# Kernel optimization log

Measured on AMD Instinct MI355X. Metric: run time of the kernel, lower is better.

## Reference

```python
import jax, jax.numpy as jnp
import numpy as np

B, S, V, E, H, L = 16, 256, 32000, 512, 1024, 2


def setup_inputs() -> dict:
    key = jax.random.key(0)
    ks = jax.random.split(key, 10)
    scale = 0.02
    tokens = jax.random.randint(ks[0], (B, S), 1, V)  # avoid pad token 0
    emb = jax.random.normal(ks[1], (V, E), dtype=jnp.float32) * scale
    W0 = jax.random.normal(ks[2], (E, 4 * H), dtype=jnp.float32) * scale
    U0 = jax.random.normal(ks[3], (H, 4 * H), dtype=jnp.float32) * scale
    b0 = jnp.zeros((4 * H,), dtype=jnp.float32)
    W1 = jax.random.normal(ks[4], (H, 4 * H), dtype=jnp.float32) * scale
    U1 = jax.random.normal(ks[5], (H, 4 * H), dtype=jnp.float32) * scale
    b1 = jnp.zeros((4 * H,), dtype=jnp.float32)
    Wd = jax.random.normal(ks[6], (H, V), dtype=jnp.float32) * scale
    bd = jnp.zeros((V,), dtype=jnp.float32)
    return {"tokens": tokens, "emb": emb, "W0": W0, "U0": U0, "b0": b0,
            "W1": W1, "U1": U1, "b1": b1, "Wd": Wd, "bd": bd}


def lstm_layer(x, mask, W, U, b):
    """Keras LSTM (gate order i,f,g,o), mask carries state/output on padded steps.
    x: [B,S,D], mask: [B,S] bool -> (ys [B,S,H], h [B,H], c [B,H])."""
    h_dim = U.shape[0]
    bsz = x.shape[0]
    x_t = jnp.swapaxes(x, 0, 1)           # [S,B,D]
    m_t = jnp.swapaxes(mask, 0, 1)        # [S,B]

    def step(carry, inp):
        h, c = carry
        xt, mt = inp
        z = xt @ W + h @ U + b            # [B,4H]
        i, f, g, o = jnp.split(z, 4, axis=-1)
        c_new = jax.nn.sigmoid(f) * c + jax.nn.sigmoid(i) * jnp.tanh(g)
        h_new = jax.nn.sigmoid(o) * jnp.tanh(c_new)
        mt = mt[:, None]
        h_new = jnp.where(mt, h_new, h)
        c_new = jnp.where(mt, c_new, c)
        return (h_new, c_new), h_new

    init = (jnp.zeros((bsz, h_dim), x.dtype), jnp.zeros((bsz, h_dim), x.dtype))
    (h, c), ys = jax.lax.scan(step, init, (x_t, m_t))
    return jnp.swapaxes(ys, 0, 1), h, c


def reference(tokens, emb, W0, U0, b0, W1, U1, b1, Wd, bd):
    mask = tokens != 0                    # mask_zero=True in Embedding
    x = emb[tokens]                       # [B,S,E]
    x, h0, c0 = lstm_layer(x, mask, W0, U0, b0)
    x, h1, c1 = lstm_layer(x, mask, W1, U1, b1)
    probs = jax.nn.softmax(x @ Wd + bd, axis=-1)  # Dense(softmax) -> [B,S,V]
    h_stack = jnp.stack([h0, h1])         # [L,B,H] final hidden states
    c_stack = jnp.stack([c0, c1])         # [L,B,H] final cell states
    return probs, h_stack, c_stack
```

## Files before the change

kernel.cpp:

```cpp
#include <hip/hip_runtime.h>

typedef __attribute__((ext_vector_type(8))) short bf16x8;
typedef __attribute__((ext_vector_type(4))) float f32x4;

#define S_LEN 256
#define VOCAB 32000
#define EMB   512
#define HID   1024

static const size_t OUT_H = 131072000ull;

__device__ inline unsigned short f2bf(float f) {
  unsigned int u = __float_as_uint(f);
  u = (u + 0x7FFFu + ((u >> 16) & 1u)) >> 16;
  return (unsigned short)u;
}

__device__ inline void st_h(unsigned short* p, unsigned short v) {
  __hip_atomic_store(p, v, __ATOMIC_RELAXED, __HIP_MEMORY_SCOPE_AGENT);
}

__device__ inline int xcd_swz(int o, int n) {
  int q = n >> 3, r = n & 7;
  int x = o & 7, i = o >> 3;
  return (x < r ? x * (q + 1) : r * (q + 1) + (x - r) * q) + i;
}

__global__ __launch_bounds__(256) void k_transpose_bf16(const float* __restrict__ src,
                                                        unsigned short* __restrict__ dst,
                                                        int K, int N) {
  __shared__ float tile[64][65];
  int n0 = blockIdx.x * 64, k0 = blockIdx.y * 64;
  int tid = threadIdx.x;
#pragma unroll
  for (int i = 0; i < 16; ++i) {
    int e = tid + i * 256;
    int r = e >> 6, c = e & 63;
    tile[r][c] = src[(size_t)(k0 + r) * N + n0 + c];
  }
  __syncthreads();
#pragma unroll
  for (int i = 0; i < 16; ++i) {
    int e = tid + i * 256;
    int r = e >> 6, c = e & 63;
    dst[(size_t)(n0 + r) * K + k0 + c] = f2bf(tile[c][r]);
  }
}

__global__ __launch_bounds__(256) void k_gather_emb(const int* __restrict__ tokens,
                                                    const float* __restrict__ emb,
                                                    unsigned short* __restrict__ Xg) {
  int r = blockIdx.x;
  int s = r >> 4, b = r & 15;
  int tok = tokens[b * S_LEN + s];
  const float* src = emb + (size_t)tok * EMB;
  int k = threadIdx.x * 2;
  float2 v = *(const float2*)(src + k);
  ushort2 o; o.x = f2bf(v.x); o.y = f2bf(v.y);
  *(ushort2*)(Xg + (size_t)r * EMB + k) = o;
}

__device__ inline void gload16(const void* g, void* lds) {
  __builtin_amdgcn_global_load_lds((const __attribute__((address_space(1))) unsigned int*)g,
                                   (__attribute__((address_space(3))) unsigned int*)lds,
                                   16, 0, 0);
}

template <bool SMPART>
__global__ __launch_bounds__(256) void k_gemm_bf16(const unsigned short* __restrict__ A,
                                                   const unsigned short* __restrict__ BT,
                                                   float* __restrict__ C,
                                                   const float* __restrict__ bias,
                                                   int M, int N, int K,
                                                   float* __restrict__ Mpart,
                                                   float* __restrict__ Spart,
                                                   int NT) {
  __shared__ unsigned short As[4096];
  __shared__ unsigned short Bs[4096];
  __shared__ float redM[2][2][64];
  __shared__ float redS[2][2][64];
  int tid = threadIdx.x;
  int lane = tid & 63, wv = tid >> 6;
  int wr = wv >> 1, wc = wv & 1;
  int bxs = xcd_swz(blockIdx.x, gridDim.x);
  int am0 = blockIdx.y * 128, bn0 = bxs * 128;
  f32x4 zero = {0.f, 0.f, 0.f, 0.f};
  f32x4 acc[4][4];
#pragma unroll
  for (int m = 0; m < 4; ++m)
#pragma unroll
    for (int n = 0; n < 4; ++n) acc[m][n] = zero;
  int KT = K >> 5;
  int lr = lane & 15, kq = lane >> 4;
  for (int kt = 0; kt < KT; ++kt) {
    int k0 = kt << 5;
    __syncthreads();
#pragma unroll
    for (int c = 0; c < 2; ++c) {
      int t2 = c * 256 + tid;
      int row = t2 & 127, kg = t2 >> 7;
      gload16(A + (size_t)(am0 + row) * K + k0 + kg * 8, &As[(c * 256 + wv * 64) * 8]);
    }
#pragma unroll
    for (int c = 0; c < 2; ++c) {
      int t2 = c * 256 + tid;
      int row = t2 & 127, kg = t2 >> 7;
      gload16(BT + (size_t)(bn0 + row) * K + k0 + kg * 8, &Bs[(c * 256 + wv * 64) * 8]);
    }
    __syncthreads();
    const bf16x8* Ap = (const bf16x8*)As;
    const bf16x8* Bp = (const bf16x8*)Bs;
    bf16x8 af[4], bf[4];
#pragma unroll
    for (int m = 0; m < 4; ++m) af[m] = Ap[kq * 128 + wr * 64 + m * 16 + lr];
#pragma unroll
    for (int n = 0; n < 4; ++n) bf[n] = Bp[kq * 128 + wc * 64 + n * 16 + lr];
#pragma unroll
    for (int m = 0; m < 4; ++m)
#pragma unroll
      for (int n = 0; n < 4; ++n)
        acc[m][n] = __builtin_amdgcn_mfma_f32_16x16x32_bf16(af[m], bf[n], acc[m][n], 0, 0, 0);
  }
  float bvc[4];
#pragma unroll
  for (int n = 0; n < 4; ++n) {
    int col = bn0 + wc * 64 + n * 16 + lr;
    bvc[n] = bias ? bias[col] : 0.f;
  }
#pragma unroll
  for (int m = 0; m < 4; ++m)
#pragma unroll
    for (int n = 0; n < 4; ++n) {
      int col = bn0 + wc * 64 + n * 16 + lr;
#pragma unroll
      for (int q = 0; q < 4; ++q) {
        int row = am0 + wr * 64 + m * 16 + kq * 4 + q;
        C[(size_t)row * N + col] = acc[m][n][q] + bvc[n];
      }
    }
  if constexpr (SMPART) {
#pragma unroll
    for (int m = 0; m < 4; ++m)
#pragma unroll
      for (int q = 0; q < 4; ++q) {
        float mx = fmaxf(fmaxf(acc[m][0][q] + bvc[0], acc[m][1][q] + bvc[1]),
                         fmaxf(acc[m][2][q] + bvc[2], acc[m][3][q] + bvc[3]));
#pragma unroll
        for (int off = 1; off < 16; off <<= 1) mx = fmaxf(mx, __shfl_xor(mx, off));
        if (lr == 0) redM[wr][wc][m * 16 + kq * 4 + q] = mx;
      }
    __syncthreads();
#pragma unroll
    for (int m = 0; m < 4; ++m)
#pragma unroll
      for (int q = 0; q < 4; ++q) {
        int idx = m * 16 + kq * 4 + q;
        float mxF = fmaxf(redM[wr][0][idx], redM[wr][1][idx]);
        float s = __expf(acc[m][0][q] + bvc[0] - mxF) + __expf(acc[m][1][q] + bvc[1] - mxF) +
                  __expf(acc[m][2][q] + bvc[2] - mxF) + __expf(acc[m][3][q] + bvc[3] - mxF);
#pragma unroll
        for (int off = 1; off < 16; off <<= 1) s += __shfl_xor(s, off);
        if (lr == 0) redS[wr][wc][idx] = s;
      }
    __syncthreads();
    if (wc == 0 && lr == 0) {
#pragma unroll
      for (int m = 0; m < 4; ++m)
#pragma unroll
        for (int q = 0; q < 4; ++q) {
          int idx = m * 16 + kq * 4 + q;
          int row = am0 + wr * 64 + idx;
          Mpart[(size_t)row * NT + bxs] = fmaxf(redM[wr][0][idx], redM[wr][1][idx]);
          Spart[(size_t)row * NT + bxs] = redS[wr][0][idx] + redS[wr][1][idx];
        }
    }
  }
}

__global__ __launch_bounds__(256) void k_sm_combine(const float* __restrict__ Mp,
                                                    const float* __restrict__ Sp,
                                                    float* __restrict__ MS, int T) {
  int row = blockIdx.x * 4 + (threadIdx.x >> 6);
  int lane = threadIdx.x & 63;
  float mx = -3.4e38f;
  for (int i = lane; i < T; i += 64) mx = fmaxf(mx, Mp[(size_t)row * T + i]);
#pragma unroll
  for (int o = 32; o > 0; o >>= 1) mx = fmaxf(mx, __shfl_xor(mx, o));
  float s = 0.f;
  for (int i = lane; i < T; i += 64)
    s += Sp[(size_t)row * T + i] * __expf(Mp[(size_t)row * T + i] - mx);
#pragma unroll
  for (int o = 32; o > 0; o >>= 1) s += __shfl_xor(s, o);
  if (lane == 0) { MS[row * 2] = mx; MS[row * 2 + 1] = 1.f / s; }
}

__global__ __launch_bounds__(256) void k_sm_apply(float* __restrict__ data,
                                                  const float* __restrict__ MS) {
  const int total = 4096 * (VOCAB / 4);
  for (int idx = blockIdx.x * 256 + threadIdx.x; idx < total; idx += gridDim.x * 256) {
    int row = idx / (VOCAB / 4);
    float M = MS[row * 2], inv = MS[row * 2 + 1];
    float4 v = ((const float4*)data)[idx];
    v.x = __expf(v.x - M) * inv;
    v.y = __expf(v.y - M) * inv;
    v.z = __expf(v.z - M) * inv;
    v.w = __expf(v.w - M) * inv;
    ((float4*)data)[idx] = v;
  }
}

struct LstmSmem {
  unsigned short U0s[16384];
  unsigned short W1s[16384];
  unsigned short U1s[16384];
  float zA[4][16][16];
  float zB[4][16][16];
  float c0[16][4], h0f[16][4], c1[16][4], h1f[16][4];
  float b1s[16];
  short toks[16][256];
};

__global__ __launch_bounds__(256, 1) void k_lstm(const int* __restrict__ tokens,
                                                 const float* __restrict__ XW,
                                                 const unsigned short* __restrict__ U0T,
                                                 const unsigned short* __restrict__ W1T,
                                                 const unsigned short* __restrict__ U1T,
                                                 const float* __restrict__ b1,
                                                 unsigned short* __restrict__ h0r,
                                                 unsigned short* __restrict__ h1r,
                                                 unsigned short* __restrict__ Y1,
                                                 float* outHC,
                                                 int* bar) {
  extern __shared__ char smraw[];
  LstmSmem& sm = *(LstmSmem*)smraw;
  int tid = threadIdx.x, bid = blockIdx.x;
  int lane = tid & 63, wv = tid >> 6;

  for (int idx = tid; idx < 2048; idx += 256) {
    int cidx = idx >> 7, kg = idx & 127;
    int gcol = (cidx >> 2) * 1024 + bid * 4 + (cidx & 3);
    *(uint4*)&sm.U0s[(kg * 16 + cidx) * 8] = *(const uint4*)&U0T[(size_t)gcol * 1024 + kg * 8];
    *(uint4*)&sm.W1s[(kg * 16 + cidx) * 8] = *(const uint4*)&W1T[(size_t)gcol * 1024 + kg * 8];
    *(uint4*)&sm.U1s[(kg * 16 + cidx) * 8] = *(const uint4*)&U1T[(size_t)gcol * 1024 + kg * 8];
  }
  for (int idx = tid; idx < 4096; idx += 256) {
    sm.toks[idx >> 8][idx & 255] = (short)tokens[idx];
  }
  if (tid < 64) {
    int b = tid >> 2, u = tid & 3;
    sm.c0[b][u] = 0.f; sm.h0f[b][u] = 0.f;
    sm.c1[b][u] = 0.f; sm.h1f[b][u] = 0.f;
  }
  if (tid < 16) sm.b1s[tid] = b1[(tid >> 2) * 1024 + bid * 4 + (tid & 3)];
  __syncthreads();

  int lr = lane & 15, kq = lane >> 4;

  auto gbar = [&](int gen) {
    __syncthreads();
    if (tid == 0)
      __hip_atomic_store(&bar[bid * 16], gen, __ATOMIC_RELAXED, __HIP_MEMORY_SCOPE_AGENT);
    int ok;
    do {
      int f = __hip_atomic_load(&bar[tid * 16], __ATOMIC_RELAXED, __HIP_MEMORY_SCOPE_AGENT);
      ok = (f >= gen);
    } while (!__syncthreads_and(ok));
  };

  if (wv == 1) {
    int l = tid - 64, b = l >> 2, u = l & 3;
    const float* xp = XW + (size_t)b * 4096 + bid * 4 + u;
    float z0 = xp[0], z1 = xp[1024], z2 = xp[2048], z3 = xp[3072];
    (void)z1;
    float ii = 1.f / (1.f + expf(-z0));
    float gg = tanhf(z2);
    float oo = 1.f / (1.f + expf(-z3));
    float cn = ii * gg;
    float hn = oo * tanhf(cn);
    if (sm.toks[b][0] == 0) { cn = 0.f; hn = 0.f; }
    sm.c0[b][u] = cn; sm.h0f[b][u] = hn;
    st_h(h0r + b * HID + bid * 4 + u, f2bf(hn));
  }
  gbar(1);

  for (int t = 0; t < 255; ++t) {
    const unsigned short* h0t = h0r + (size_t)t * 16384;
    const unsigned short* h1p = h1r + (size_t)(t > 0 ? t - 1 : 0) * 16384;
    unsigned short* h1c = h1r + (size_t)t * 16384;
    unsigned short* h0n = h0r + (size_t)(t + 1) * 16384;

    float xwv0 = 0, xwv1 = 0, xwv2 = 0, xwv3 = 0;
    if (wv == 1) {
      int l = tid - 64, b = l >> 2, u = l & 3;
      const float* xp = XW + ((size_t)(t + 1) * 16 + b) * 4096 + bid * 4 + u;
      xwv0 = xp[0]; xwv1 = xp[1024]; xwv2 = xp[2048]; xwv3 = xp[3072];
    }

    f32x4 accB = {0.f, 0.f, 0.f, 0.f};
    {
      const unsigned short* ap = (wv < 2) ? h0t : h1p;
      const unsigned short* bm = (wv < 2) ? sm.W1s : sm.U1s;
      int kofs = (wv & 1) * 512;
      if (wv < 2 || t > 0) {
#pragma unroll
        for (int s8 = 0; s8 < 16; ++s8) {
          int kb = kofs + s8 * 32;
          bf16x8 av = *(const bf16x8*)(ap + lr * HID + kb + kq * 8);
          bf16x8 bv = *(const bf16x8*)&bm[(((kb >> 3) + kq) * 16 + lr) * 8];
          accB = __builtin_amdgcn_mfma_f32_16x16x32_bf16(av, bv, accB, 0, 0, 0);
        }
      }
    }
    f32x4 accA = {0.f, 0.f, 0.f, 0.f};
#pragma unroll
    for (int s8 = 0; s8 < 8; ++s8) {
      int kb = wv * 256 + s8 * 32;
      bf16x8 av = *(const bf16x8*)(h0t + lr * HID + kb + kq * 8);
      bf16x8 bv = *(const bf16x8*)&sm.U0s[(((kb >> 3) + kq) * 16 + lr) * 8];
      accA = __builtin_amdgcn_mfma_f32_16x16x32_bf16(av, bv, accA, 0, 0, 0);
    }
#pragma unroll
    for (int q = 0; q < 4; ++q) {
      sm.zB[wv][kq * 4 + q][lr] = accB[q];
      sm.zA[wv][kq * 4 + q][lr] = accA[q];
    }
    __syncthreads();

    if (wv == 0) {
      int b = tid >> 2, u = tid & 3;
      int tok = sm.toks[b][t];
      float z0 = sm.b1s[0 + u]  + sm.zB[0][b][0 + u]  + sm.zB[1][b][0 + u]  + sm.zB[2][b][0 + u]  + sm.zB[3][b][0 + u];
      float z1 = sm.b1s[4 + u]  + sm.zB[0][b][4 + u]  + sm.zB[1][b][4 + u]  + sm.zB[2][b][4 + u]  + sm.zB[3][b][4 + u];
      float z2 = sm.b1s[8 + u]  + sm.zB[0][b][8 + u]  + sm.zB[1][b][8 + u]  + sm.zB[2][b][8 + u]  + sm.zB[3][b][8 + u];
      float z3 = sm.b1s[12 + u] + sm.zB[0][b][12 + u] + sm.zB[1][b][12 + u] + sm.zB[2][b][12 + u] + sm.zB[3][b][12 + u];
      float ii = 1.f / (1.f + expf(-z0));
      float ff = 1.f / (1.f + expf(-z1));
      float gg = tanhf(z2);
      float oo = 1.f / (1.f + expf(-z3));
      float cold = sm.c1[b][u], hold = sm.h1f[b][u];
      float cn = ff * cold + ii * gg;
      float hn = oo * tanhf(cn);
      if (tok == 0) { cn = cold; hn = hold; }
      sm.c1[b][u] = cn; sm.h1f[b][u] = hn;
      unsigned short hb = f2bf(hn);
      st_h(h1c + b * HID + bid * 4 + u, hb);
      Y1[((size_t)b * S_LEN + t) * HID + bid * 4 + u] = hb;
    } else if (wv == 1) {
      int l = tid - 64, b = l >> 2, u = l & 3;
      int tok = sm.toks[b][t + 1];
      float z0 = xwv0 + sm.zA[0][b][0 + u]  + sm.zA[1][b][0 + u]  + sm.zA[2][b][0 + u]  + sm.zA[3][b][0 + u];
      float z1 = xwv1 + sm.zA[0][b][4 + u]  + sm.zA[1][b][4 + u]  + sm.zA[2][b][4 + u]  + sm.zA[3][b][4 + u];
      float z2 = xwv2 + sm.zA[0][b][8 + u]  + sm.zA[1][b][8 + u]  + sm.zA[2][b][8 + u]  + sm.zA[3][b][8 + u];
      float z3 = xwv3 + sm.zA[0][b][12 + u] + sm.zA[1][b][12 + u] + sm.zA[2][b][12 + u] + sm.zA[3][b][12 + u];
      float ii = 1.f / (1.f + expf(-z0));
      float ff = 1.f / (1.f + expf(-z1));
      float gg = tanhf(z2);
      float oo = 1.f / (1.f + expf(-z3));
      float cold = sm.c0[b][u], hold = sm.h0f[b][u];
      float cn = ff * cold + ii * gg;
      float hn = oo * tanhf(cn);
      if (tok == 0) { cn = cold; hn = hold; }
      sm.c0[b][u] = cn; sm.h0f[b][u] = hn;
      st_h(h0n + b * HID + bid * 4 + u, f2bf(hn));
    }
    gbar(t + 2);
  }

  {
    const unsigned short* h0t = h0r + 255ull * 16384;
    const unsigned short* h1p = h1r + 254ull * 16384;
    f32x4 accB = {0.f, 0.f, 0.f, 0.f};
    const unsigned short* ap = (wv < 2) ? h0t : h1p;
    const unsigned short* bm = (wv < 2) ? sm.W1s : sm.U1s;
    int kofs = (wv & 1) * 512;
#pragma unroll
    for (int s8 = 0; s8 < 16; ++s8) {
      int kb = kofs + s8 * 32;
      bf16x8 av = *(const bf16x8*)(ap + lr * HID + kb + kq * 8);
      bf16x8 bv = *(const bf16x8*)&bm[(((kb >> 3) + kq) * 16 + lr) * 8];
      accB = __builtin_amdgcn_mfma_f32_16x16x32_bf16(av, bv, accB, 0, 0, 0);
    }
#pragma unroll
    for (int q = 0; q < 4; ++q) sm.zB[wv][kq * 4 + q][lr] = accB[q];
    __syncthreads();
    if (wv == 0) {
      int b = tid >> 2, u = tid & 3;
      int tok = sm.toks[b][255];
      float z0 = sm.b1s[0 + u]  + sm.zB[0][b][0 + u]  + sm.zB[1][b][0 + u]  + sm.zB[2][b][0 + u]  + sm.zB[3][b][0 + u];
      float z1 = sm.b1s[4 + u]  + sm.zB[0][b][4 + u]  + sm.zB[1][b][4 + u]  + sm.zB[2][b][4 + u]  + sm.zB[3][b][4 + u];
      float z2 = sm.b1s[8 + u]  + sm.zB[0][b][8 + u]  + sm.zB[1][b][8 + u]  + sm.zB[2][b][8 + u]  + sm.zB[3][b][8 + u];
      float z3 = sm.b1s[12 + u] + sm.zB[0][b][12 + u] + sm.zB[1][b][12 + u] + sm.zB[2][b][12 + u] + sm.zB[3][b][12 + u];
      float ii = 1.f / (1.f + expf(-z0));
      float ff = 1.f / (1.f + expf(-z1));
      float gg = tanhf(z2);
      float oo = 1.f / (1.f + expf(-z3));
      float cold = sm.c1[b][u], hold = sm.h1f[b][u];
      float cn = ff * cold + ii * gg;
      float hn = oo * tanhf(cn);
      if (tok == 0) { cn = cold; hn = hold; }
      sm.c1[b][u] = cn; sm.h1f[b][u] = hn;
      Y1[((size_t)b * S_LEN + 255) * HID + bid * 4 + u] = f2bf(hn);
    }
    __syncthreads();
  }

  if (tid < 64) {
    int b = tid >> 2, u = tid & 3, ug = bid * 4 + u;
    outHC[OUT_H + (size_t)b * HID + ug]         = sm.h0f[b][u];
    outHC[OUT_H + 16384 + (size_t)b * HID + ug] = sm.h1f[b][u];
    outHC[OUT_H + 32768 + (size_t)b * HID + ug] = sm.c0[b][u];
    outHC[OUT_H + 49152 + (size_t)b * HID + ug] = sm.c1[b][u];
  }
}

extern "C" void kernel_launch(void* const* d_in, const int* in_sizes, int n_in,
                              void* d_out, int out_size, void* d_ws, size_t ws_size,
                              hipStream_t stream) {
  const int*   tokens = (const int*)d_in[0];
  const float* emb = (const float*)d_in[1];
  const float* W0  = (const float*)d_in[2];
  const float* U0  = (const float*)d_in[3];
  const float* b0  = (const float*)d_in[4];
  const float* W1  = (const float*)d_in[5];
  const float* U1  = (const float*)d_in[6];
  const float* b1  = (const float*)d_in[7];
  const float* Wd  = (const float*)d_in[8];
  const float* bd  = (const float*)d_in[9];
  float* out = (float*)d_out;

  char* ws = (char*)d_ws;
  size_t off = 0;
  auto alloc = [&](size_t bytes) { char* p = ws + off; off += (bytes + 255) & ~(size_t)255; return p; };
  unsigned short* W0T = (unsigned short*)alloc(4096ull * 512 * 2);
  unsigned short* U0T = (unsigned short*)alloc(4096ull * 1024 * 2);
  unsigned short* W1T = (unsigned short*)alloc(4096ull * 1024 * 2);
  unsigned short* U1T = (unsigned short*)alloc(4096ull * 1024 * 2);
  unsigned short* WdT = (unsigned short*)alloc(32000ull * 1024 * 2);
  unsigned short* Xg  = (unsigned short*)alloc(4096ull * 512 * 2);
  unsigned short* Y1  = (unsigned short*)alloc(4096ull * 1024 * 2);
  int*   bar   = (int*)alloc(16384);
  float* Mpart = (float*)alloc(4096ull * 250 * 4);
  float* Spart = (float*)alloc(4096ull * 250 * 4);
  float* MS    = (float*)alloc(4096ull * 2 * 4);

  float* XW = out;
  unsigned short* h0r = (unsigned short*)((char*)d_out + 192ull * 1024 * 1024);
  unsigned short* h1r = (unsigned short*)((char*)d_out + 208ull * 1024 * 1024);

  hipMemsetAsync(bar, 0, 16384, stream);

  hipFuncSetAttribute((const void*)k_lstm, hipFuncAttributeMaxDynamicSharedMemorySize,
                      (int)sizeof(LstmSmem));

  k_transpose_bf16<<<dim3(64, 8), 256, 0, stream>>>(W0, W0T, 512, 4096);
  k_transpose_bf16<<<dim3(64, 16), 256, 0, stream>>>(U0, U0T, 1024, 4096);
  k_transpose_bf16<<<dim3(64, 16), 256, 0, stream>>>(W1, W1T, 1024, 4096);
  k_transpose_bf16<<<dim3(64, 16), 256, 0, stream>>>(U1, U1T, 1024, 4096);
  k_transpose_bf16<<<dim3(500, 16), 256, 0, stream>>>(Wd, WdT, 1024, 32000);
  k_gather_emb<<<4096, 256, 0, stream>>>(tokens, emb, Xg);

  k_gemm_bf16<false><<<dim3(32, 32), 256, 0, stream>>>(Xg, W0T, XW, b0, 4096, 4096, 512,
                                                       nullptr, nullptr, 0);

  k_lstm<<<256, 256, sizeof(LstmSmem), stream>>>(tokens, XW, U0T, W1T, U1T, b1,
                                                 h0r, h1r, Y1, out, bar);

  k_gemm_bf16<true><<<dim3(250, 32), 256, 0, stream>>>(Y1, WdT, out, bd, 4096, 32000, 1024,
                                                       Mpart, Spart, 250);
  k_sm_combine<<<1024, 256, 0, stream>>>(Mpart, Spart, MS, 250);
  k_sm_apply<<<4096, 256, 0, stream>>>(out, MS);
}
```

Measured before the change: 2.423 ms.

## Split LSTM recurrence into two batch-half phases and store logits in bf16

The persistent LSTM kernel now handles the batch as two halves of 8 rows, each with its own grid-wide flag array. One half's compute can then overlap with other blocks still publishing the other half, which loosens the single global barrier per timestep. The MFMA A-operand rows are folded (r8) so each phase reads only 8 batch rows. Separately, when the workspace is large enough, the vocab GEMM writes bf16 logits to a scratch buffer and a new softmax-apply kernel reads them back, halving the logits round-trip traffic at the cost of bf16 rounding of the logits before exponentiation.

```diff
diff --git a/kernel.cpp b/kernel.cpp
--- a/kernel.cpp
+++ b/kernel.cpp
@@ -14,6 +14,9 @@
   unsigned int u = __float_as_uint(f);
   u = (u + 0x7FFFu + ((u >> 16) & 1u)) >> 16;
   return (unsigned short)u;
+}
+__device__ inline float bf2f(unsigned short s) {
+  return __uint_as_float(((unsigned int)s) << 16);
 }
 
 __device__ inline void st_h(unsigned short* p, unsigned short v) {
@@ -66,10 +69,11 @@
                                    16, 0, 0);
 }
 
-template <bool SMPART>
+template <bool SMPART, bool BF16OUT>
 __global__ __launch_bounds__(256) void k_gemm_bf16(const unsigned short* __restrict__ A,
                                                    const unsigned short* __restrict__ BT,
-                                                   float* __restrict__ C,
+                                                   float* __restrict__ Cf,
+                                                   unsigned short* __restrict__ Cb,
                                                    const float* __restrict__ bias,
                                                    int M, int N, int K,
                                                    float* __restrict__ Mpart,
@@ -135,7 +139,10 @@
 #pragma unroll
       for (int q = 0; q < 4; ++q) {
         int row = am0 + wr * 64 + m * 16 + kq * 4 + q;
-        C[(size_t)row * N + col] = acc[m][n][q] + bvc[n];
+        if constexpr (BF16OUT)
+          Cb[(size_t)row * N + col] = f2bf(acc[m][n][q] + bvc[n]);
+        else
+          Cf[(size_t)row * N + col] = acc[m][n][q] + bvc[n];
       }
     }
   if constexpr (SMPART) {
@@ -206,6 +213,23 @@
     v.z = __expf(v.z - M) * inv;
     v.w = __expf(v.w - M) * inv;
     ((float4*)data)[idx] = v;
+  }
+}
+
+__global__ __launch_bounds__(256) void k_sm_apply_bf16(const unsigned short* __restrict__ lg,
+                                                       float* __restrict__ probs,
+                                                       const float* __restrict__ MS) {
+  const int total = 4096 * (VOCAB / 4);
+  for (int idx = blockIdx.x * 256 + threadIdx.x; idx < total; idx += gridDim.x * 256) {
+    int row = idx / (VOCAB / 4);
+    float M = MS[row * 2], inv = MS[row * 2 + 1];
+    ushort4 v = ((const ushort4*)lg)[idx];
+    float4 o;
+    o.x = __expf(bf2f(v.x) - M) * inv;
+    o.y = __expf(bf2f(v.y) - M) * inv;
+    o.z = __expf(bf2f(v.z) - M) * inv;
+    o.w = __expf(bf2f(v.w) - M) * inv;
+    ((float4*)probs)[idx] = o;
   }
 }
 
@@ -255,14 +279,19 @@
   __syncthreads();
 
   int lr = lane & 15, kq = lane >> 4;
-
-  auto gbar = [&](int gen) {
+  int r8 = lane & 7;
+  int* flag0 = bar;
+  int* flag1 = bar + 4096;
+
+  auto publish = [&](int* base, int gen) {
     __syncthreads();
     if (tid == 0)
-      __hip_atomic_store(&bar[bid * 16], gen, __ATOMIC_RELAXED, __HIP_MEMORY_SCOPE_AGENT);
+      __hip_atomic_store(&base[bid * 16], gen, __ATOMIC_RELAXED, __HIP_MEMORY_SCOPE_AGENT);
+  };
+  auto wait_flags = [&](int* base, int gen) {
     int ok;
     do {
-      int f = __hip_atomic_load(&bar[tid * 16], __ATOMIC_RELAXED, __HIP_MEMORY_SCOPE_AGENT);
+      int f = __hip_atomic_load(&base[tid * 16], __ATOMIC_RELAXED, __HIP_MEMORY_SCOPE_AGENT);
       ok = (f >= gen);
     } while (!__syncthreads_and(ok));
   };
@@ -270,8 +299,7 @@
   if (wv == 1) {
     int l = tid - 64, b = l >> 2, u = l & 3;
     const float* xp = XW + (size_t)b * 4096 + bid * 4 + u;
-    float z0 = xp[0], z1 = xp[1024], z2 = xp[2048], z3 = xp[3072];
-    (void)z1;
+    float z0 = xp[0], z2 = xp[2048], z3 = xp[3072];
     float ii = 1.f / (1.f + expf(-z0));
     float gg = tanhf(z2);
     float oo = 1.f / (1.f + expf(-z3));
@@ -281,17 +309,18 @@
     sm.c0[b][u] = cn; sm.h0f[b][u] = hn;
     st_h(h0r + b * HID + bid * 4 + u, f2bf(hn));
   }
-  gbar(1);
-
-  for (int t = 0; t < 255; ++t) {
-    const unsigned short* h0t = h0r + (size_t)t * 16384;
-    const unsigned short* h1p = h1r + (size_t)(t > 0 ? t - 1 : 0) * 16384;
-    unsigned short* h1c = h1r + (size_t)t * 16384;
-    unsigned short* h0n = h0r + (size_t)(t + 1) * 16384;
+  publish(flag0, 1);
+  publish(flag1, 1);
+
+  auto phase = [&](int ph, int t) {
+    const unsigned short* h0t = h0r + (size_t)t * 16384 + ph * 8192;
+    const unsigned short* h1p = h1r + (size_t)(t > 0 ? t - 1 : 0) * 16384 + ph * 8192;
+    unsigned short* h1c = h1r + (size_t)t * 16384 + ph * 8192;
+    unsigned short* h0n = h0r + (size_t)(t + 1) * 16384 + ph * 8192;
 
     float xwv0 = 0, xwv1 = 0, xwv2 = 0, xwv3 = 0;
-    if (wv == 1) {
-      int l = tid - 64, b = l >> 2, u = l & 3;
+    if (wv == 1 && lane < 32) {
+      int b = ph * 8 + (lane >> 2), u = lane & 3;
       const float* xp = XW + ((size_t)(t + 1) * 16 + b) * 4096 + bid * 4 + u;
       xwv0 = xp[0]; xwv1 = xp[1024]; xwv2 = xp[2048]; xwv3 = xp[3072];
     }
@@ -305,7 +334,7 @@
 #pragma unroll
         for (int s8 = 0; s8 < 16; ++s8) {
           int kb = kofs + s8 * 32;
-          bf16x8 av = *(const bf16x8*)(ap + lr * HID + kb + kq * 8);
+          bf16x8 av = *(const bf16x8*)(ap + r8 * HID + kb + kq * 8);
           bf16x8 bv = *(const bf16x8*)&bm[(((kb >> 3) + kq) * 16 + lr) * 8];
           accB = __builtin_amdgcn_mfma_f32_16x16x32_bf16(av, bv, accB, 0, 0, 0);
         }
@@ -315,7 +344,7 @@
 #pragma unroll
     for (int s8 = 0; s8 < 8; ++s8) {
       int kb = wv * 256 + s8 * 32;
-      bf16x8 av = *(const bf16x8*)(h0t + lr * HID + kb + kq * 8);
+      bf16x8 av = *(const bf16x8*)(h0t + r8 * HID + kb + kq * 8);
       bf16x8 bv = *(const bf16x8*)&sm.U0s[(((kb >> 3) + kq) * 16 + lr) * 8];
       accA = __builtin_amdgcn_mfma_f32_16x16x32_bf16(av, bv, accA, 0, 0, 0);
     }
@@ -326,13 +355,13 @@
     }
     __syncthreads();
 
-    if (wv == 0) {
-      int b = tid >> 2, u = tid & 3;
+    if (tid < 32) {
+      int bl = tid >> 2, u = tid & 3, b = ph * 8 + bl;
       int tok = sm.toks[b][t];
-      float z0 = sm.b1s[0 + u]  + sm.zB[0][b][0 + u]  + sm.zB[1][b][0 + u]  + sm.zB[2][b][0 + u]  + sm.zB[3][b][0 + u];
-      float z1 = sm.b1s[4 + u]  + sm.zB[0][b][4 + u]  + sm.zB[1][b][4 + u]  + sm.zB[2][b][4 + u]  + sm.zB[3][b][4 + u];
-      float z2 = sm.b1s[8 + u]  + sm.zB[0][b][8 + u]  + sm.zB[1][b][8 + u]  + sm.zB[2][b][8 + u]  + sm.zB[3][b][8 + u];
-      float z3 = sm.b1s[12 + u] + sm.zB[0][b][12 + u] + sm.zB[1][b][12 + u] + sm.zB[2][b][12 + u] + sm.zB[3][b][12 + u];
+      float z0 = sm.b1s[0 + u]  + sm.zB[0][bl][0 + u]  + sm.zB[1][bl][0 + u]  + sm.zB[2][bl][0 + u]  + sm.zB[3][bl][0 + u];
+      float z1 = sm.b1s[4 + u]  + sm.zB[0][bl][4 + u]  + sm.zB[1][bl][4 + u]  + sm.zB[2][bl][4 + u]  + sm.zB[3][bl][4 + u];
+      float z2 = sm.b1s[8 + u]  + sm.zB[0][bl][8 + u]  + sm.zB[1][bl][8 + u]  + sm.zB[2][bl][8 + u]  + sm.zB[3][bl][8 + u];
+      float z3 = sm.b1s[12 + u] + sm.zB[0][bl][12 + u] + sm.zB[1][bl][12 + u] + sm.zB[2][bl][12 + u] + sm.zB[3][bl][12 + u];
       float ii = 1.f / (1.f + expf(-z0));
       float ff = 1.f / (1.f + expf(-z1));
       float gg = tanhf(z2);
@@ -343,15 +372,15 @@
       if (tok == 0) { cn = cold; hn = hold; }
       sm.c1[b][u] = cn; sm.h1f[b][u] = hn;
       unsigned short hb = f2bf(hn);
-      st_h(h1c + b * HID + bid * 4 + u, hb);
+      st_h(h1c + bl * HID + bid * 4 + u, hb);
       Y1[((size_t)b * S_LEN + t) * HID + bid * 4 + u] = hb;
-    } else if (wv == 1) {
-      int l = tid - 64, b = l >> 2, u = l & 3;
+    } else if (wv == 1 && lane < 32) {
+      int bl = lane >> 2, u = lane & 3, b = ph * 8 + bl;
       int tok = sm.toks[b][t + 1];
-      float z0 = xwv0 + sm.zA[0][b][0 + u]  + sm.zA[1][b][0 + u]  + sm.zA[2][b][0 + u]  + sm.zA[3][b][0 + u];
-      float z1 = xwv1 + sm.zA[0][b][4 + u]  + sm.zA[1][b][4 + u]  + sm.zA[2][b][4 + u]  + sm.zA[3][b][4 + u];
-      float z2 = xwv2 + sm.zA[0][b][8 + u]  + sm.zA[1][b][8 + u]  + sm.zA[2][b][8 + u]  + sm.zA[3][b][8 + u];
-      float z3 = xwv3 + sm.zA[0][b][12 + u] + sm.zA[1][b][12 + u] + sm.zA[2][b][12 + u] + sm.zA[3][b][12 + u];
+      float z0 = xwv0 + sm.zA[0][bl][0 + u]  + sm.zA[1][bl][0 + u]  + sm.zA[2][bl][0 + u]  + sm.zA[3][bl][0 + u];
+      float z1 = xwv1 + sm.zA[0][bl][4 + u]  + sm.zA[1][bl][4 + u]  + sm.zA[2][bl][4 + u]  + sm.zA[3][bl][4 + u];
+      float z2 = xwv2 + sm.zA[0][bl][8 + u]  + sm.zA[1][bl][8 + u]  + sm.zA[2][bl][8 + u]  + sm.zA[3][bl][8 + u];
+      float z3 = xwv3 + sm.zA[0][bl][12 + u] + sm.zA[1][bl][12 + u] + sm.zA[2][bl][12 + u] + sm.zA[3][bl][12 + u];
       float ii = 1.f / (1.f + expf(-z0));
       float ff = 1.f / (1.f + expf(-z1));
       float gg = tanhf(z2);
@@ -361,14 +390,22 @@
       float hn = oo * tanhf(cn);
       if (tok == 0) { cn = cold; hn = hold; }
       sm.c0[b][u] = cn; sm.h0f[b][u] = hn;
-      st_h(h0n + b * HID + bid * 4 + u, f2bf(hn));
-    }
-    gbar(t + 2);
-  }
-
-  {
-    const unsigned short* h0t = h0r + 255ull * 16384;
-    const unsigned short* h1p = h1r + 254ull * 16384;
+      st_h(h0n + bl * HID + bid * 4 + u, f2bf(hn));
+    }
+  };
+
+  for (int t = 0; t < 255; ++t) {
+    wait_flags(flag0, t + 1);
+    phase(0, t);
+    publish(flag0, t + 2);
+    wait_flags(flag1, t + 1);
+    phase(1, t);
+    publish(flag1, t + 2);
+  }
+
+  auto phaseEp = [&](int ph) {
+    const unsigned short* h0t = h0r + 255ull * 16384 + ph * 8192;
+    const unsigned short* h1p = h1r + 254ull * 16384 + ph * 8192;
     f32x4 accB = {0.f, 0.f, 0.f, 0.f};
     const unsigned short* ap = (wv < 2) ? h0t : h1p;
     const unsigned short* bm = (wv < 2) ? sm.W1s : sm.U1s;
@@ -376,20 +413,20 @@
 #pragma unroll
     for (int s8 = 0; s8 < 16; ++s8) {
       int kb = kofs + s8 * 32;
-      bf16x8 av = *(const bf16x8*)(ap + lr * HID + kb + kq * 8);
+      bf16x8 av = *(const bf16x8*)(ap + r8 * HID + kb + kq * 8);
       bf16x8 bv = *(const bf16x8*)&bm[(((kb >> 3) + kq) * 16 + lr) * 8];
       accB = __builtin_amdgcn_mfma_f32_16x16x32_bf16(av, bv, accB, 0, 0, 0);
     }
 #pragma unroll
     for (int q = 0; q < 4; ++q) sm.zB[wv][kq * 4 + q][lr] = accB[q];
     __syncthreads();
-    if (wv == 0) {
-      int b = tid >> 2, u = tid & 3;
+    if (tid < 32) {
+      int bl = tid >> 2, u = tid & 3, b = ph * 8 + bl;
       int tok = sm.toks[b][255];
-      float z0 = sm.b1s[0 + u]  + sm.zB[0][b][0 + u]  + sm.zB[1][b][0 + u]  + sm.zB[2][b][0 + u]  + sm.zB[3][b][0 + u];
-      float z1 = sm.b1s[4 + u]  + sm.zB[0][b][4 + u]  + sm.zB[1][b][4 + u]  + sm.zB[2][b][4 + u]  + sm.zB[3][b][4 + u];
-      float z2 = sm.b1s[8 + u]  + sm.zB[0][b][8 + u]  + sm.zB[1][b][8 + u]  + sm.zB[2][b][8 + u]  + sm.zB[3][b][8 + u];
-      float z3 = sm.b1s[12 + u] + sm.zB[0][b][12 + u] + sm.zB[1][b][12 + u] + sm.zB[2][b][12 + u] + sm.zB[3][b][12 + u];
+      float z0 = sm.b1s[0 + u]  + sm.zB[0][bl][0 + u]  + sm.zB[1][bl][0 + u]  + sm.zB[2][bl][0 + u]  + sm.zB[3][bl][0 + u];
+      float z1 = sm.b1s[4 + u]  + sm.zB[0][bl][4 + u]  + sm.zB[1][bl][4 + u]  + sm.zB[2][bl][4 + u]  + sm.zB[3][bl][4 + u];
+      float z2 = sm.b1s[8 + u]  + sm.zB[0][bl][8 + u]  + sm.zB[1][bl][8 + u]  + sm.zB[2][bl][8 + u]  + sm.zB[3][bl][8 + u];
+      float z3 = sm.b1s[12 + u] + sm.zB[0][bl][12 + u] + sm.zB[1][bl][12 + u] + sm.zB[2][bl][12 + u] + sm.zB[3][bl][12 + u];
       float ii = 1.f / (1.f + expf(-z0));
       float ff = 1.f / (1.f + expf(-z1));
       float gg = tanhf(z2);
@@ -402,7 +439,11 @@
       Y1[((size_t)b * S_LEN + 255) * HID + bid * 4 + u] = f2bf(hn);
     }
     __syncthreads();
-  }
+  };
+  wait_flags(flag0, 256);
+  phaseEp(0);
+  wait_flags(flag1, 256);
+  phaseEp(1);
 
   if (tid < 64) {
     int b = tid >> 2, u = tid & 3, ug = bid * 4 + u;
@@ -438,16 +479,19 @@
   unsigned short* WdT = (unsigned short*)alloc(32000ull * 1024 * 2);
   unsigned short* Xg  = (unsigned short*)alloc(4096ull * 512 * 2);
   unsigned short* Y1  = (unsigned short*)alloc(4096ull * 1024 * 2);
-  int*   bar   = (int*)alloc(16384);
+  int*   bar   = (int*)alloc(32768);
   float* Mpart = (float*)alloc(4096ull * 250 * 4);
   float* Spart = (float*)alloc(4096ull * 250 * 4);
   float* MS    = (float*)alloc(4096ull * 2 * 4);
+  unsigned short* Lb = nullptr;
+  if (ws_size >= off + 4096ull * VOCAB * 2 + 256)
+    Lb = (unsigned short*)alloc(4096ull * VOCAB * 2);
 
   float* XW = out;
   unsigned short* h0r = (unsigned short*)((char*)d_out + 192ull * 1024 * 1024);
   unsigned short* h1r = (unsigned short*)((char*)d_out + 208ull * 1024 * 1024);
 
-  hipMemsetAsync(bar, 0, 16384, stream);
+  hipMemsetAsync(bar, 0, 32768, stream);
 
   hipFuncSetAttribute((const void*)k_lstm, hipFuncAttributeMaxDynamicSharedMemorySize,
                       (int)sizeof(LstmSmem));
@@ -459,14 +503,24 @@
   k_transpose_bf16<<<dim3(500, 16), 256, 0, stream>>>(Wd, WdT, 1024, 32000);
   k_gather_emb<<<4096, 256, 0, stream>>>(tokens, emb, Xg);
 
-  k_gemm_bf16<false><<<dim3(32, 32), 256, 0, stream>>>(Xg, W0T, XW, b0, 4096, 4096, 512,
-                                                       nullptr, nullptr, 0);
+  k_gemm_bf16<false, false><<<dim3(32, 32), 256, 0, stream>>>(Xg, W0T, XW, nullptr, b0,
+                                                              4096, 4096, 512,
+                                                              nullptr, nullptr, 0);
 
   k_lstm<<<256, 256, sizeof(LstmSmem), stream>>>(tokens, XW, U0T, W1T, U1T, b1,
                                                  h0r, h1r, Y1, out, bar);
 
-  k_gemm_bf16<true><<<dim3(250, 32), 256, 0, stream>>>(Y1, WdT, out, bd, 4096, 32000, 1024,
-                                                       Mpart, Spart, 250);
-  k_sm_combine<<<1024, 256, 0, stream>>>(Mpart, Spart, MS, 250);
-  k_sm_apply<<<4096, 256, 0, stream>>>(out, MS);
-}
+  if (Lb) {
+    k_gemm_bf16<true, true><<<dim3(250, 32), 256, 0, stream>>>(Y1, WdT, nullptr, Lb, bd,
+                                                               4096, 32000, 1024,
+                                                               Mpart, Spart, 250);
+    k_sm_combine<<<1024, 256, 0, stream>>>(Mpart, Spart, MS, 250);
+    k_sm_apply_bf16<<<4096, 256, 0, stream>>>(Lb, out, MS);
+  } else {
+    k_gemm_bf16<true, false><<<dim3(250, 32), 256, 0, stream>>>(Y1, WdT, out, nullptr, bd,
+                                                                4096, 32000, 1024,
+                                                                Mpart, Spart, 250);
+    k_sm_combine<<<1024, 256, 0, stream>>>(Mpart, Spart, MS, 250);
+    k_sm_apply<<<4096, 256, 0, stream>>>(out, MS);
+  }
+}
```

Result: slower. 3.094 ms (+27.7%).

## Store logits as bf16 scratch and batch LSTM hidden-state stores

Applied to the files above, without the earlier changes.

The vocab GEMM now writes its logits into a bf16 workspace buffer instead of the fp32 output. A new softmax-apply kernel reads that bf16 buffer and writes fp32 probabilities, so the logit write and re-read move half the bytes. The code falls back to the old path when the workspace is too small. Separately, the LSTM stages each block's hidden-state bf16 values in shared memory and publishes them with one 64-bit atomic store per batch row, instead of scalar 16-bit stores. This adds a __syncthreads per step and rounds the logits to bf16 before exp, which loses some precision.

```diff
diff --git a/kernel.cpp b/kernel.cpp
--- a/kernel.cpp
+++ b/kernel.cpp
@@ -14,6 +14,9 @@
   unsigned int u = __float_as_uint(f);
   u = (u + 0x7FFFu + ((u >> 16) & 1u)) >> 16;
   return (unsigned short)u;
+}
+__device__ inline float bf2f(unsigned short s) {
+  return __uint_as_float(((unsigned int)s) << 16);
 }
 
 __device__ inline void st_h(unsigned short* p, unsigned short v) {
@@ -66,10 +69,11 @@
                                    16, 0, 0);
 }
 
-template <bool SMPART>
+template <bool SMPART, bool BF16OUT>
 __global__ __launch_bounds__(256) void k_gemm_bf16(const unsigned short* __restrict__ A,
                                                    const unsigned short* __restrict__ BT,
-                                                   float* __restrict__ C,
+                                                   float* __restrict__ Cf,
+                                                   unsigned short* __restrict__ Cb,
                                                    const float* __restrict__ bias,
                                                    int M, int N, int K,
                                                    float* __restrict__ Mpart,
@@ -135,7 +139,10 @@
 #pragma unroll
       for (int q = 0; q < 4; ++q) {
         int row = am0 + wr * 64 + m * 16 + kq * 4 + q;
-        C[(size_t)row * N + col] = acc[m][n][q] + bvc[n];
+        if constexpr (BF16OUT)
+          Cb[(size_t)row * N + col] = f2bf(acc[m][n][q] + bvc[n]);
+        else
+          Cf[(size_t)row * N + col] = acc[m][n][q] + bvc[n];
       }
     }
   if constexpr (SMPART) {
@@ -209,6 +216,23 @@
   }
 }
 
+__global__ __launch_bounds__(256) void k_sm_apply_bf16(const unsigned short* __restrict__ lg,
+                                                       float* __restrict__ probs,
+                                                       const float* __restrict__ MS) {
+  const int total = 4096 * (VOCAB / 4);
+  for (int idx = blockIdx.x * 256 + threadIdx.x; idx < total; idx += gridDim.x * 256) {
+    int row = idx / (VOCAB / 4);
+    float M = MS[row * 2], inv = MS[row * 2 + 1];
+    ushort4 v = ((const ushort4*)lg)[idx];
+    float4 o;
+    o.x = __expf(bf2f(v.x) - M) * inv;
+    o.y = __expf(bf2f(v.y) - M) * inv;
+    o.z = __expf(bf2f(v.z) - M) * inv;
+    o.w = __expf(bf2f(v.w) - M) * inv;
+    ((float4*)probs)[idx] = o;
+  }
+}
+
 struct LstmSmem {
   unsigned short U0s[16384];
   unsigned short W1s[16384];
@@ -218,6 +242,7 @@
   float c0[16][4], h0f[16][4], c1[16][4], h1f[16][4];
   float b1s[16];
   short toks[16][256];
+  unsigned short h0st[16][4], h1st[16][4];
 };
 
 __global__ __launch_bounds__(256, 1) void k_lstm(const int* __restrict__ tokens,
@@ -270,8 +295,7 @@
   if (wv == 1) {
     int l = tid - 64, b = l >> 2, u = l & 3;
     const float* xp = XW + (size_t)b * 4096 + bid * 4 + u;
-    float z0 = xp[0], z1 = xp[1024], z2 = xp[2048], z3 = xp[3072];
-    (void)z1;
+    float z0 = xp[0], z2 = xp[2048], z3 = xp[3072];
     float ii = 1.f / (1.f + expf(-z0));
     float gg = tanhf(z2);
     float oo = 1.f / (1.f + expf(-z3));
@@ -343,7 +367,7 @@
       if (tok == 0) { cn = cold; hn = hold; }
       sm.c1[b][u] = cn; sm.h1f[b][u] = hn;
       unsigned short hb = f2bf(hn);
-      st_h(h1c + b * HID + bid * 4 + u, hb);
+      sm.h1st[b][u] = hb;
       Y1[((size_t)b * S_LEN + t) * HID + bid * 4 + u] = hb;
     } else if (wv == 1) {
       int l = tid - 64, b = l >> 2, u = l & 3;
@@ -361,7 +385,17 @@
       float hn = oo * tanhf(cn);
       if (tok == 0) { cn = cold; hn = hold; }
       sm.c0[b][u] = cn; sm.h0f[b][u] = hn;
-      st_h(h0n + b * HID + bid * 4 + u, f2bf(hn));
+      sm.h0st[b][u] = f2bf(hn);
+    }
+    __syncthreads();
+    if (tid < 32) {
+      int b = tid & 15;
+      unsigned long long v = *(const unsigned long long*)((tid < 16) ? &sm.h1st[b][0]
+                                                                     : &sm.h0st[b][0]);
+      unsigned short* dst = (tid < 16) ? (h1c + b * HID + bid * 4)
+                                       : (h0n + b * HID + bid * 4);
+      __hip_atomic_store((unsigned long long*)dst, v, __ATOMIC_RELAXED,
+                         __HIP_MEMORY_SCOPE_AGENT);
     }
     gbar(t + 2);
   }
@@ -442,6 +476,9 @@
   float* Mpart = (float*)alloc(4096ull * 250 * 4);
   float* Spart = (float*)alloc(4096ull * 250 * 4);
   float* MS    = (float*)alloc(4096ull * 2 * 4);
+  unsigned short* Lb = nullptr;
+  if (ws_size >= off + 4096ull * VOCAB * 2 + 256)
+    Lb = (unsigned short*)alloc(4096ull * VOCAB * 2);
 
   float* XW = out;
   unsigned short* h0r = (unsigned short*)((char*)d_out + 192ull * 1024 * 1024);
@@ -459,14 +496,24 @@
   k_transpose_bf16<<<dim3(500, 16), 256, 0, stream>>>(Wd, WdT, 1024, 32000);
   k_gather_emb<<<4096, 256, 0, stream>>>(tokens, emb, Xg);
 
-  k_gemm_bf16<false><<<dim3(32, 32), 256, 0, stream>>>(Xg, W0T, XW, b0, 4096, 4096, 512,
-                                                       nullptr, nullptr, 0);
+  k_gemm_bf16<false, false><<<dim3(32, 32), 256, 0, stream>>>(Xg, W0T, XW, nullptr, b0,
+                                                              4096, 4096, 512,
+                                                              nullptr, nullptr, 0);
 
   k_lstm<<<256, 256, sizeof(LstmSmem), stream>>>(tokens, XW, U0T, W1T, U1T, b1,
                                                  h0r, h1r, Y1, out, bar);
 
-  k_gemm_bf16<true><<<dim3(250, 32), 256, 0, stream>>>(Y1, WdT, out, bd, 4096, 32000, 1024,
-                                                       Mpart, Spart, 250);
-  k_sm_combine<<<1024, 256, 0, stream>>>(Mpart, Spart, MS, 250);
-  k_sm_apply<<<4096, 256, 0, stream>>>(out, MS);
-}
+  if (Lb) {
+    k_gemm_bf16<true, true><<<dim3(250, 32), 256, 0, stream>>>(Y1, WdT, nullptr, Lb, bd,
+                                                               4096, 32000, 1024,
+                                                               Mpart, Spart, 250);
+    k_sm_combine<<<1024, 256, 0, stream>>>(Mpart, Spart, MS, 250);
+    k_sm_apply_bf16<<<4096, 256, 0, stream>>>(Lb, out, MS);
+  } else {
+    k_gemm_bf16<true, false><<<dim3(250, 32), 256, 0, stream>>>(Y1, WdT, out, nullptr, bd,
+                                                                4096, 32000, 1024,
+                                                                Mpart, Spart, 250);
+    k_sm_combine<<<1024, 256, 0, stream>>>(Mpart, Spart, MS, 250);
+    k_sm_apply<<<4096, 256, 0, stream>>>(out, MS);
+  }
+}
```

New measurement: 2.363 ms. -2.5%, faster.
